# Kernel optimization log

Measured on AMD Instinct MI355X. Metric: run time of the kernel, lower is better.

The kernel has to match this reference:

```python
import jax, jax.numpy as jnp
import numpy as np

GROUP_NUMS = 30
T_ITERS = 10
SIGMA = 0.01
SEED_THRESHOLD = 0.1


def _gumbel_topk(key, logits, k):
    # Sampling without replacement (torch.multinomial replacement=False) via Gumbel-top-k.
    u = jax.random.uniform(key, logits.shape, minval=1e-9, maxval=1.0)
    g = -jnp.log(-jnp.log(u))
    return jax.lax.top_k(logits + g, k)[1]


def _pairwise_dist(x):
    # x: [B,3,S] -> [B,S,S]
    return jnp.linalg.norm(x[:, :, :, None] - x[:, :, None, :], axis=1)


def _one_iterate(key, src_xyz, src_corr_xyz, weights, seed_nums, group_nums):
    B, _, N = src_xyz.shape
    S, G = seed_nums, group_nums
    k1, k2 = jax.random.split(key)
    # seed sampling without replacement, proportional to weights
    seed_idx = _gumbel_topk(k1, jnp.log(weights), S)                       # [B,S]
    seed_w = jnp.take_along_axis(weights, seed_idx, axis=-1)              # [B,S]
    idx3 = jnp.broadcast_to(seed_idx[:, None, :], (B, 3, S))
    seed_src = jnp.take_along_axis(src_xyz, idx3, axis=-1)                # [B,3,S]
    seed_corr = jnp.take_along_axis(src_corr_xyz, idx3, axis=-1)          # [B,3,S]
    # geometric consensus (no_grad in torch)
    cons = jnp.exp(-(_pairwise_dist(seed_src) - _pairwise_dist(seed_corr)) ** 2 / SIGMA)
    cons = jax.lax.stop_gradient(jnp.clip(cons, 0.1, None))               # [B,S,S]
    probs = cons / jnp.sum(cons, axis=-1, keepdims=True)
    nn_idx = _gumbel_topk(k2, jnp.log(probs), G)                          # [B,S,G]
    bidx = jnp.arange(B)[:, None, None]
    src_pts = seed_src.transpose(0, 2, 1)                                 # [B,S,3]
    corr_pts = seed_corr.transpose(0, 2, 1)
    src_nn = src_pts[bidx, nn_idx]                                        # [B,S,G,3]
    corr_nn = corr_pts[bidx, nn_idx]                                      # [B,S,G,3]
    w_nn = seed_w[bidx, nn_idx]                                           # [B,S,G]
    src2 = src_nn.transpose(0, 1, 3, 2).reshape(B * S, 3, G)
    corr2 = corr_nn.transpose(0, 1, 3, 2).reshape(B * S, 3, G)
    w2 = w_nn.reshape(B * S, G)
    w2 = w2 / jnp.sum(w2, axis=-1, keepdims=True)
    src_c = src2 - src2.mean(axis=2, keepdims=True)
    corr_c = corr2 - corr2.mean(axis=2, keepdims=True)
    H = jnp.matmul(src_c * w2[:, None, :], corr_c.transpose(0, 2, 1))     # [BS,3,3]
    U, _, Vh = jnp.linalg.svd(H)
    V = Vh.transpose(0, 2, 1)          # torch.svd returns V (not V^T)
    Ut = U.transpose(0, 2, 1)
    detv = jnp.linalg.det(jnp.matmul(V, Ut))                              # [BS]
    d = jnp.stack([jnp.ones_like(detv), jnp.ones_like(detv), detv], axis=-1)
    R = jnp.matmul(V * d[:, None, :], Ut)                                 # V @ diag(1,1,det) @ U^T
    t = jnp.matmul(-R, src2.mean(axis=2, keepdims=True)) + corr2.mean(axis=2, keepdims=True)  # [BS,3,1]
    R = R.reshape(B, S, 3, 3)
    t = t.reshape(B, S, 1, 3)
    pred = jnp.einsum('bsnm,bmk->bsnk', R, src_xyz) + t.transpose(0, 1, 3, 2)  # [B,S,3,N]
    L2 = jnp.linalg.norm(pred - src_corr_xyz[:, None, :, :], axis=-2)     # [B,S,N]
    fitness = jnp.mean((L2 < SEED_THRESHOLD).astype(jnp.float32), axis=-1)  # [B,S]
    best = jnp.argmax(fitness, axis=-1)                                   # [B]
    vv = jnp.mean(jnp.max(fitness, axis=-1))
    ba = jnp.arange(B)
    return vv, R[ba, best], t[ba, best]


def setup_inputs() -> dict:
    key = jax.random.key(0)
    k1, k2, k3 = jax.random.split(key, 3)
    B, N = 8, 2048
    src_xyz = jax.random.normal(k1, (B, 3, N), dtype=jnp.float32)
    tgt_xyz = jax.random.normal(k2, (B, 3, N), dtype=jnp.float32)
    weights = jax.random.normal(k3, (B, N), dtype=jnp.float32)
    return {"src_xyz": src_xyz, "tgt_xyz": tgt_xyz, "weights": weights}


def reference(src_xyz, tgt_xyz, weights):
    key = jax.random.key(42)
    w = jnp.where(jnp.isnan(weights), jnp.float32(1e-7), weights)
    w = jnp.where(jnp.isinf(w), jnp.float32(1.0), w)
    seed_nums = w.shape[-1] // 2
    w = jax.nn.softmax(w, axis=-1)
    B = src_xyz.shape[0]
    dist = jnp.float32(1e8)
    Rs = jnp.zeros((B, 3, 3), jnp.float32)
    ts = jnp.zeros((B, 1, 3), jnp.float32)
    for it in range(T_ITERS):
        vv, fR, ft = _one_iterate(jax.random.fold_in(key, it), src_xyz, tgt_xyz, w, seed_nums, GROUP_NUMS)
        better = vv < dist
        Rs = jnp.where(better, fR, Rs)
        ts = jnp.where(better, ft, ts)
        dist = jnp.where(better, vv, dist)
    return Rs, ts[:, 0, :]
```

## Files before the change

kernel.cpp:

```cpp
#include <hip/hip_runtime.h>
#include <stdint.h>
#include <math.h>

#pragma clang fp contract(off)

#define NB    8
#define NPTS  2048
#define NS    1024
#define NG    30
#define NITER 10

typedef unsigned long long ull;

__host__ __device__ __forceinline__ uint32_t rotl32(uint32_t x, int r){
  return (x << r) | (x >> (32 - r));
}
__host__ __device__ __forceinline__ void tf2x32(uint32_t k0, uint32_t k1,
                                                uint32_t x0, uint32_t x1,
                                                uint32_t& o0, uint32_t& o1){
  uint32_t k2 = k0 ^ k1 ^ 0x1BD11BDAu;
  x0 += k0; x1 += k1;
#define TFR(r) { x0 += x1; x1 = rotl32(x1, (r)); x1 ^= x0; }
  TFR(13) TFR(15) TFR(26) TFR(6)
  x0 += k1; x1 += k2 + 1u;
  TFR(17) TFR(29) TFR(16) TFR(24)
  x0 += k2; x1 += k0 + 2u;
  TFR(13) TFR(15) TFR(26) TFR(6)
  x0 += k0; x1 += k1 + 3u;
  TFR(17) TFR(29) TFR(16) TFR(24)
  x0 += k1; x1 += k2 + 4u;
  TFR(13) TFR(15) TFR(26) TFR(6)
  x0 += k2; x1 += k0 + 5u;
#undef TFR
  o0 = x0; o1 = x1;
}

__device__ __forceinline__ uint32_t rand_bits(uint32_t k0, uint32_t k1, uint32_t e){
  uint32_t o0, o1; tf2x32(k0, k1, 0u, e, o0, o1);
  return o0 ^ o1;
}

__device__ __forceinline__ void derive_key(int it, uint32_t which,
                                           uint32_t& a, uint32_t& b){
  uint32_t fa, fb;
  tf2x32(0u, 42u, 0u, (uint32_t)it, fa, fb);
  tf2x32(fa, fb, 0u, which, a, b);
}

__device__ __forceinline__ float gumbel_from(uint32_t bits){
  float f = __uint_as_float((bits >> 9) | 0x3f800000u) - 1.0f;
  float u = fmaxf(1e-9f, f + 1e-9f);
  return -logf(-logf(u));
}

__device__ __forceinline__ ull packkey(float v, uint32_t idx){
  uint32_t u = __float_as_uint(v);
  u = (u & 0x80000000u) ? ~u : (u | 0x80000000u);
  return ((ull)u << 32) | (ull)(0xFFFFFFFFu - idx);
}
__device__ __forceinline__ uint32_t unpackidx(ull k){
  return 0xFFFFFFFFu - (uint32_t)(k & 0xFFFFFFFFull);
}

__device__ __forceinline__ void bitonic_desc(ull* a, int M, int t, int T){
  for (int k = 2; k <= M; k <<= 1){
    for (int j = k >> 1; j > 0; j >>= 1){
      for (int i = t; i < M; i += T){
        int ixj = i ^ j;
        if (ixj > i){
          ull ai = a[i], aj = a[ixj];
          bool desc = ((i & k) == 0);
          if (desc ? (ai < aj) : (ai > aj)){ a[i] = aj; a[ixj] = ai; }
        }
      }
      __syncthreads();
    }
  }
}

__device__ __forceinline__ ull shfl_xor_u64(ull x, int mask){
  return (ull)__shfl_xor((long long)x, mask, 64);
}

__device__ __forceinline__ ull sort32_desc(ull key, int l){
  int i = l & 31;
#pragma unroll
  for (int k = 2; k <= 16; k <<= 1){
#pragma unroll
    for (int j = k >> 1; j > 0; j >>= 1){
      ull other = shfl_xor_u64(key, j);
      bool up = ((l & j) == 0);
      bool take_max = (((i & k) == 0) == up);
      bool omax = other > key;
      key = (take_max == omax) ? other : key;
    }
  }
#pragma unroll
  for (int j = 16; j > 0; j >>= 1){
    ull other = shfl_xor_u64(key, j);
    bool up = ((l & j) == 0);
    bool omax = other > key;
    key = (up == omax) ? other : key;
  }
  return key;
}

__device__ __forceinline__ ull merge64_desc(ull key, int l){
#pragma unroll
  for (int j = 32; j > 0; j >>= 1){
    ull other = shfl_xor_u64(key, j);
    bool up = ((l & j) == 0);
    bool omax = other > key;
    key = (up == omax) ? other : key;
  }
  return key;
}

__device__ __forceinline__ ull mergehalves_desc(ull key, int l){
  ull rev = shfl_xor_u64(key, 31);
  if (l >= 32) key = rev;
  return merge64_desc(key, l);
}

__global__ __launch_bounds__(256) void ghv_softmax(const float* __restrict__ win,
                                                   float* __restrict__ w,
                                                   float* __restrict__ logw){
  int b = blockIdx.x, t = threadIdx.x;
  __shared__ float sh[NPTS];
  __shared__ float red[4];
  __shared__ float bcast;
  for (int n = t; n < NPTS; n += 256){
    float x = win[b*NPTS + n];
    if (isnan(x)) x = 1e-7f;
    if (isinf(x)) x = 1.0f;
    sh[n] = x;
  }
  __syncthreads();
  float m = -INFINITY;
  for (int n = t; n < NPTS; n += 256) m = fmaxf(m, sh[n]);
  for (int off = 32; off >= 1; off >>= 1) m = fmaxf(m, __shfl_down(m, off));
  if ((t & 63) == 0) red[t >> 6] = m;
  __syncthreads();
  if (t == 0) bcast = fmaxf(fmaxf(red[0], red[1]), fmaxf(red[2], red[3]));
  __syncthreads();
  float mx = bcast;
  float ss = 0.0f;
  for (int n = t; n < NPTS; n += 256){ float e = expf(sh[n] - mx); sh[n] = e; ss += e; }
  for (int off = 32; off >= 1; off >>= 1) ss += __shfl_down(ss, off);
  if ((t & 63) == 0) red[t >> 6] = ss;
  __syncthreads();
  if (t == 0) bcast = red[0] + red[1] + red[2] + red[3];
  __syncthreads();
  float tot = bcast;
  for (int n = t; n < NPTS; n += 256){
    float wv = sh[n] / tot;
    w[b*NPTS + n] = wv;
    logw[b*NPTS + n] = logf(wv);
  }
}

__global__ __launch_bounds__(1024) void ghv_seed(const float* __restrict__ src,
                                                 const float* __restrict__ tgt,
                                                 const float* __restrict__ w,
                                                 const float* __restrict__ logw,
                                                 float* __restrict__ seeds,
                                                 int it0, int seq){
  __shared__ ull keys[NPTS];
  __shared__ uint32_t kk[2];
  int b = blockIdx.x, t = threadIdx.x;
  int it = it0 + blockIdx.z;
  int slot = seq ? 0 : it;
  if (t == 0){ derive_key(it, 0u, kk[0], kk[1]); }
  __syncthreads();
  uint32_t k0 = kk[0], k1 = kk[1];
  for (int n = t; n < NPTS; n += 1024){
    uint32_t bits = rand_bits(k0, k1, (uint32_t)(b*NPTS + n));
    float v = logw[b*NPTS + n] + gumbel_from(bits);
    keys[n] = packkey(v, (uint32_t)n);
  }
  __syncthreads();
  bitonic_desc(keys, NPTS, t, 1024);
  int s = t;
  uint32_t idx = unpackidx(keys[s]);
  const float* sb = src + b*3*NPTS;
  const float* tb = tgt + b*3*NPTS;
  float* sp = seeds + (size_t)slot*(NB*NS*8) + (size_t)((b << 10) + s) * 8;
  sp[0] = sb[idx]; sp[1] = sb[NPTS + idx]; sp[2] = sb[2*NPTS + idx];
  sp[3] = tb[idx]; sp[4] = tb[NPTS + idx]; sp[5] = tb[2*NPTS + idx];
  sp[6] = w[b*NPTS + idx]; sp[7] = 0.0f;
}

__global__ __launch_bounds__(512) void ghv_nn(const float* __restrict__ seeds,
                                              unsigned short* __restrict__ nnb,
                                              int it0, int seq){
  __shared__ float red[8];
  __shared__ float srow[8];
  __shared__ float rowsum_sh;
  __shared__ float cmax[32];
  __shared__ float Tsh;
  __shared__ int cnt_sh;
  __shared__ uint32_t kk[2];
  __shared__ ull kbuf[NS];
  __shared__ ull sbuf[256];
  __shared__ ull sbuf2[128];

  int s = blockIdx.x, b = blockIdx.y, t = threadIdx.x;
  int it = it0 + blockIdx.z;
  int slot = seq ? 0 : it;
  const float* sdat = seeds + (size_t)slot*(NB*NS*8);
  size_t outoff = ((size_t)slot*(NB*NS) + (size_t)((b << 10) + s))*32;
  int wv = t >> 6, l = t & 63;

  if (t < 8) srow[t] = sdat[(size_t)((b << 10) + s)*8 + t];
  if (t == 0){ derive_key(it, 1u, kk[0], kk[1]); cnt_sh = 0; }
  __syncthreads();
  uint32_t k0 = kk[0], k1 = kk[1];

  float consr[2];
  float part = 0.0f;
#pragma unroll
  for (int q = 0; q < 2; ++q){
    int j = t + q*512;
    const float4* jp = (const float4*)(sdat + (size_t)((b << 10) + j)*8);
    float4 p0 = jp[0], p1 = jp[1];
    float dxs = srow[0]-p0.x, dys = srow[1]-p0.y, dzs = srow[2]-p0.z;
    float ds  = sqrtf(dxs*dxs + dys*dys + dzs*dzs);
    float dxc = srow[3]-p0.w, dyc = srow[4]-p1.x, dzc = srow[5]-p1.y;
    float dc  = sqrtf(dxc*dxc + dyc*dyc + dzc*dzc);
    float diff = ds - dc;
    float cons = expf((-(diff*diff)) / 0.01f);
    cons = fmaxf(cons, 0.1f);
    consr[q] = cons;
    part += cons;
  }
  for (int off = 32; off >= 1; off >>= 1) part += __shfl_down(part, off);
  if ((t & 63) == 0) red[t >> 6] = part;
  __syncthreads();
  if (t == 0){ float tot = 0.0f; for (int i = 0; i < 8; ++i) tot += red[i]; rowsum_sh = tot; }
  __syncthreads();
  float rowsum = rowsum_sh;

  float v0, v1; ull key0, key1;
  {
    int e = t;
    uint32_t bits = rand_bits(k0, k1, (uint32_t)((b << 20) + (s << 10) + e));
    v0 = logf(consr[0] / rowsum) + gumbel_from(bits);
    key0 = packkey(v0, (uint32_t)e);
  }
  {
    int e = t + 512;
    uint32_t bits = rand_bits(k0, k1, (uint32_t)((b << 20) + (s << 10) + e));
    v1 = logf(consr[1] / rowsum) + gumbel_from(bits);
    key1 = packkey(v1, (uint32_t)e);
  }

  {
    float cm0 = v0;
#pragma unroll
    for (int j = 1; j <= 16; j <<= 1) cm0 = fmaxf(cm0, __shfl_xor(cm0, j));
    if ((l & 31) == 0) cmax[(wv << 1) + (l >> 5)] = cm0;
    float cm1 = v1;
#pragma unroll
    for (int j = 1; j <= 16; j <<= 1) cm1 = fmaxf(cm1, __shfl_xor(cm1, j));
    if ((l & 31) == 0) cmax[16 + (wv << 1) + (l >> 5)] = cm1;
  }
  __syncthreads();
  if (t < 32){
    float m = cmax[t];
#pragma unroll
    for (int j = 1; j <= 16; j <<= 1) m = fminf(m, __shfl_xor(m, j));
    if (t == 0) Tsh = m;
  }
  __syncthreads();
  float T = Tsh;

  bool kp0 = (v0 >= T), kp1 = (v1 >= T);
  ull b0m = __ballot(kp0), b1m = __ballot(kp1);
  int c0 = __popcll(b0m);
  int base = 0;
  if (l == 0) base = atomicAdd(&cnt_sh, c0 + __popcll(b1m));
  base = __shfl(base, 0);
  ull ltm = (l == 0) ? 0ull : ((1ull << l) - 1ull);
  if (kp0) kbuf[base + __popcll(b0m & ltm)] = key0;
  if (kp1) kbuf[base + c0 + __popcll(b1m & ltm)] = key1;
  __syncthreads();
  int n = cnt_sh;

  if (n <= 512){
    if (t >= n) kbuf[t] = 0ull;
    __syncthreads();
    ull key = 0ull;
    if (wv * 64 < n){
      key = kbuf[t];
      key = sort32_desc(key, l);
      key = mergehalves_desc(key, l);
    }
    if (l < 32) sbuf[(wv << 5) + l] = key;
    __syncthreads();
    if (wv < 4){
      ull k2 = 0ull;
      if (wv * 128 < n){
        k2 = (l < 32) ? sbuf[(wv << 6) + l] : sbuf[(wv << 6) + 95 - l];
        k2 = merge64_desc(k2, l);
      }
      if (l < 32) sbuf2[(wv << 5) + l] = k2;
    }
    __syncthreads();
    if (wv < 2){
      ull k2 = (l < 32) ? sbuf2[(wv << 6) + l] : sbuf2[(wv << 6) + 95 - l];
      k2 = merge64_desc(k2, l);
      if (l < 32) sbuf[(wv << 5) + l] = k2;
    }
    __syncthreads();
    if (wv == 0){
      ull k2 = (l < 32) ? sbuf[l] : sbuf[95 - l];
      k2 = merge64_desc(k2, l);
      if (l < 32){
        unsigned short vidx = (l < NG) ? (unsigned short)unpackidx(k2) : 0;
        nnb[outoff + l] = vidx;
      }
    }
  } else {
    kbuf[t] = key0;
    kbuf[t + 512] = key1;
    __syncthreads();
    bitonic_desc(kbuf, NS, t, 512);
    if (t < 32){
      unsigned short vidx = (t < NG) ? (unsigned short)unpackidx(kbuf[t]) : 0;
      nnb[outoff + t] = vidx;
    }
  }
}

__global__ __launch_bounds__(64) void ghv_kabsch(const float* __restrict__ seeds,
                                                 const unsigned short* __restrict__ nnb,
                                                 float* __restrict__ Rt,
                                                 int it0, int seq){
  int id = blockIdx.x*64 + threadIdx.x;
  int it = it0 + blockIdx.z;
  int slot = seq ? 0 : it;
  int b = id >> 10;
  const float* sdat = seeds + (size_t)slot*(NB*NS*8);
  const unsigned short* nnp = nnb + ((size_t)slot*(NB*NS) + (size_t)id)*32;

  float sxs=0, sys=0, szs=0, cxs=0, cys=0, czs=0, wsum=0;
  for (int g = 0; g < NG; ++g){
    int j = nnp[g];
    const float4* jp = (const float4*)(sdat + (size_t)((b << 10) + j)*8);
    float4 p0 = jp[0], p1 = jp[1];
    sxs += p0.x; sys += p0.y; szs += p0.z;
    cxs += p0.w; cys += p1.x; czs += p1.y;
    wsum += p1.z;
  }
  float msx = sxs/30.0f, msy = sys/30.0f, msz = szs/30.0f;
  float mcx = cxs/30.0f, mcy = cys/30.0f, mcz = czs/30.0f;

  float Hf[9] = {0,0,0,0,0,0,0,0,0};
  for (int g = 0; g < NG; ++g){
    int j = nnp[g];
    const float4* jp = (const float4*)(sdat + (size_t)((b << 10) + j)*8);
    float4 p0 = jp[0], p1 = jp[1];
    float wg = p1.z / wsum;
    float a0 = p0.x - msx, a1 = p0.y - msy, a2 = p0.z - msz;
    float b0 = p0.w - mcx, b1 = p1.x - mcy, b2 = p1.y - mcz;
    float a0w = a0*wg, a1w = a1*wg, a2w = a2*wg;
    Hf[0] += a0w*b0; Hf[1] += a0w*b1; Hf[2] += a0w*b2;
    Hf[3] += a1w*b0; Hf[4] += a1w*b1; Hf[5] += a1w*b2;
    Hf[6] += a2w*b0; Hf[7] += a2w*b1; Hf[8] += a2w*b2;
  }

  double H[9]; for (int i = 0; i < 9; ++i) H[i] = (double)Hf[i];
  double A[3][3];
  A[0][0] = H[0]*H[0] + H[3]*H[3] + H[6]*H[6];
  A[0][1] = H[0]*H[1] + H[3]*H[4] + H[6]*H[7];
  A[0][2] = H[0]*H[2] + H[3]*H[5] + H[6]*H[8];
  A[1][1] = H[1]*H[1] + H[4]*H[4] + H[7]*H[7];
  A[1][2] = H[1]*H[2] + H[4]*H[5] + H[7]*H[8];
  A[2][2] = H[2]*H[2] + H[5]*H[5] + H[8]*H[8];
  A[1][0] = A[0][1]; A[2][0] = A[0][2]; A[2][1] = A[1][2];
  double V[3][3] = {{1,0,0},{0,1,0},{0,0,1}};
  for (int sw = 0; sw < 12; ++sw){
    for (int p = 0; p < 2; ++p){
      for (int q = p+1; q < 3; ++q){
        double apq = A[p][q];
        if (fabs(apq) > 1e-300){
          double th = (A[q][q] - A[p][p]) / (2.0*apq);
          double tt = copysign(1.0, th) / (fabs(th) + sqrt(1.0 + th*th));
          double c  = 1.0 / sqrt(1.0 + tt*tt), sn = tt*c;
          int r = 3 - p - q;
          double app = A[p][p], aqq = A[q][q];
          double arp = A[r][p], arq = A[r][q];
          A[p][p] = app - tt*apq;
          A[q][q] = aqq + tt*apq;
          A[p][q] = 0.0; A[q][p] = 0.0;
          A[r][p] = c*arp - sn*arq; A[p][r] = A[r][p];
          A[r][q] = sn*arp + c*arq; A[q][r] = A[r][q];
          for (int kk = 0; kk < 3; ++kk){
            double vp = V[kk][p], vq = V[kk][q];
            V[kk][p] = c*vp - sn*vq;
            V[kk][q] = sn*vp + c*vq;
          }
        }
      }
    }
  }
  int o0 = 0, o1 = 1, o2 = 2;
  double l0 = A[0][0], l1 = A[1][1], l2 = A[2][2];
  double tmp; int ti;
  if (l0 < l1){ tmp=l0; l0=l1; l1=tmp; ti=o0; o0=o1; o1=ti; }
  if (l0 < l2){ tmp=l0; l0=l2; l2=tmp; ti=o0; o0=o2; o2=ti; }
  if (l1 < l2){ tmp=l1; l1=l2; l2=tmp; ti=o1; o1=o2; o2=ti; }
  double v0[3] = {V[0][o0], V[1][o0], V[2][o0]};
  double v1[3] = {V[0][o1], V[1][o1], V[2][o1]};
  double v2[3] = {V[0][o2], V[1][o2], V[2][o2]};

  double u0[3], u1[3], u2[3];
  for (int i = 0; i < 3; ++i) u0[i] = H[i*3+0]*v0[0] + H[i*3+1]*v0[1] + H[i*3+2]*v0[2];
  double n0 = sqrt(u0[0]*u0[0] + u0[1]*u0[1] + u0[2]*u0[2]);
  if (n0 > 1e-150){ u0[0]/=n0; u0[1]/=n0; u0[2]/=n0; }
  else { u0[0]=1; u0[1]=0; u0[2]=0; }
  for (int i = 0; i < 3; ++i) u1[i] = H[i*3+0]*v1[0] + H[i*3+1]*v1[1] + H[i*3+2]*v1[2];
  double d01 = u0[0]*u1[0] + u0[1]*u1[1] + u0[2]*u1[2];
  for (int i = 0; i < 3; ++i) u1[i] -= d01*u0[i];
  double n1 = sqrt(u1[0]*u1[0] + u1[1]*u1[1] + u1[2]*u1[2]);
  if (n1 > 1e-150){ u1[0]/=n1; u1[1]/=n1; u1[2]/=n1; }
  else {
    double ax = fabs(u0[0]), ay = fabs(u0[1]), az = fabs(u0[2]);
    double e[3] = {0,0,0};
    if (ax <= ay && ax <= az) e[0] = 1; else if (ay <= az) e[1] = 1; else e[2] = 1;
    double de = u0[0]*e[0] + u0[1]*e[1] + u0[2]*e[2];
    for (int i = 0; i < 3; ++i) u1[i] = e[i] - de*u0[i];
    double nn1 = sqrt(u1[0]*u1[0] + u1[1]*u1[1] + u1[2]*u1[2]);
    for (int i = 0; i < 3; ++i) u1[i] /= nn1;
  }
  u2[0] = u0[1]*u1[2] - u0[2]*u1[1];
  u2[1] = u0[2]*u1[0] - u0[0]*u1[2];
  u2[2] = u0[0]*u1[1] - u0[1]*u1[0];
  double detV = v0[0]*(v1[1]*v2[2] - v1[2]*v2[1])
              - v0[1]*(v1[0]*v2[2] - v1[2]*v2[0])
              + v0[2]*(v1[0]*v2[1] - v1[1]*v2[0]);
  float Rf[9];
  for (int i = 0; i < 3; ++i)
    for (int j = 0; j < 3; ++j)
      Rf[i*3+j] = (float)(v0[i]*u0[j] + v1[i]*u1[j] + detV*(v2[i]*u2[j]));
  float tx = -(Rf[0]*msx + Rf[1]*msy + Rf[2]*msz) + mcx;
  float ty = -(Rf[3]*msx + Rf[4]*msy + Rf[5]*msz) + mcy;
  float tz = -(Rf[6]*msx + Rf[7]*msy + Rf[8]*msz) + mcz;
  float* o = Rt + ((size_t)slot*(NB*NS) + (size_t)id)*12;
  for (int i = 0; i < 9; ++i) o[i] = Rf[i];
  o[9] = tx; o[10] = ty; o[11] = tz;
}

__global__ __launch_bounds__(256) void ghv_fitness(const float* __restrict__ src,
                                                   const float* __restrict__ tgt,
                                                   const float* __restrict__ Rt,
                                                   int* __restrict__ fit){
  __shared__ float Pf[12288];
  int b = blockIdx.y, t = threadIdx.x;
  int slot = blockIdx.z;
  int s0 = blockIdx.x * 16;
  const float4* g4s = (const float4*)(src + (size_t)b*3*NPTS);
  const float4* g4t = (const float4*)(tgt + (size_t)b*3*NPTS);
  float4* l4 = (float4*)Pf;
  for (int i = t; i < 1536; i += 256){
    l4[i] = g4s[i];
    l4[1536 + i] = g4t[i];
  }
  __syncthreads();
  int wv = t >> 6, l = t & 63;
  for (int k = 0; k < 4; ++k){
    int s = s0 + wv*4 + k;
    size_t id = (size_t)slot*(NB*NS) + (size_t)((b << 10) + s);
    const float* rt = Rt + id*12;
    float R0 = rt[0], R1 = rt[1], R2 = rt[2];
    float R3 = rt[3], R4 = rt[4], R5 = rt[5];
    float R6 = rt[6], R7 = rt[7], R8 = rt[8];
    float t0 = rt[9], t1 = rt[10], t2 = rt[11];
    int cnt = 0;
    for (int n = l; n < NPTS; n += 64){
      float x = Pf[n], y = Pf[2048 + n], z = Pf[4096 + n];
      float px = R0*x + R1*y + R2*z + t0;
      float py = R3*x + R4*y + R5*z + t1;
      float pz = R6*x + R7*y + R8*z + t2;
      float dx = px - Pf[6144 + n], dy = py - Pf[8192 + n], dz = pz - Pf[10240 + n];
      float l2 = sqrtf(dx*dx + dy*dy + dz*dz);
      cnt += (l2 < 0.1f) ? 1 : 0;
    }
    for (int off = 32; off >= 1; off >>= 1) cnt += __shfl_down(cnt, off);
    if (l == 0) fit[id] = cnt;
  }
}

__global__ __launch_bounds__(512) void ghv_select_b(const float* __restrict__ Rt,
                                                    const int* __restrict__ fit,
                                                    float* __restrict__ out){
  __shared__ int mc[NITER*NB], mi[NITER*NB];
  __shared__ int best_sh;
  int t = threadIdx.x;
  int w = t >> 6, l = t & 63;
  for (int task = w; task < NITER*NB; task += 8){
    int it = task >> 3, b = task & 7;
    int bc = -1, bi = 0;
    const int* fp = fit + (size_t)it*(NB*NS) + (b << 10);
    for (int s = l; s < NS; s += 64){
      int c = fp[s];
      if (c > bc){ bc = c; bi = s; }
    }
    for (int off = 32; off >= 1; off >>= 1){
      int oc = __shfl_down(bc, off);
      int oi = __shfl_down(bi, off);
      if (oc > bc || (oc == bc && oi < bi)){ bc = oc; bi = oi; }
    }
    if (l == 0){ mc[task] = bc; mi[task] = bi; }
  }
  __syncthreads();
  if (t == 0){
    float dist = 1e8f;
    int best = 0;
    for (int it = 0; it < NITER; ++it){
      int sum = 0;
      for (int b = 0; b < NB; ++b) sum += mc[(it << 3) + b];
      float vv = (float)sum / 16384.0f;
      if (vv < dist){ dist = vv; best = it; }
    }
    best_sh = best;
  }
  __syncthreads();
  int bit = best_sh;
  for (int i = t; i < 96; i += 512){
    float v;
    if (i < 72){
      int bb = i / 9, k = i % 9;
      v = Rt[((size_t)bit*(NB*NS) + (size_t)((bb << 10) + mi[(bit << 3) + bb]))*12 + k];
    } else {
      int ii = i - 72; int bb = ii / 3, k = ii % 3;
      v = Rt[((size_t)bit*(NB*NS) + (size_t)((bb << 10) + mi[(bit << 3) + bb]))*12 + 9 + k];
    }
    out[i] = v;
  }
}

__global__ __launch_bounds__(512) void ghv_select_s(const float* __restrict__ Rt,
                                                    const int* __restrict__ fit,
                                                    float* __restrict__ dist_ws,
                                                    float* __restrict__ out,
                                                    int first){
  __shared__ int mc[8], mi[8];
  __shared__ int flag;
  int t = threadIdx.x;
  int b = t >> 6, lane = t & 63;
  int bc = -1, bi = 0;
  for (int s = lane; s < NS; s += 64){
    int c = fit[(b << 10) + s];
    if (c > bc){ bc = c; bi = s; }
  }
  for (int off = 32; off >= 1; off >>= 1){
    int oc = __shfl_down(bc, off);
    int oi = __shfl_down(bi, off);
    if (oc > bc || (oc == bc && oi < bi)){ bc = oc; bi = oi; }
  }
  if (lane == 0){ mc[b] = bc; mi[b] = bi; }
  __syncthreads();
  if (t == 0){
    int sum = 0; for (int i = 0; i < 8; ++i) sum += mc[i];
    float vv = (float)sum / 16384.0f;
    float dist = first ? 1e8f : dist_ws[0];
    int better = (vv < dist) ? 1 : 0;
    if (better) dist_ws[0] = vv;
    flag = better;
  }
  __syncthreads();
  if (flag){
    for (int i = t; i < 96; i += 512){
      float v;
      if (i < 72){
        int bb = i / 9, k = i % 9;
        v = Rt[(size_t)((bb << 10) + mi[bb])*12 + k];
      } else {
        int ii = i - 72; int bb = ii / 3, k = ii % 3;
        v = Rt[(size_t)((bb << 10) + mi[bb])*12 + 9 + k];
      }
      out[i] = v;
    }
  }
}

extern "C" void kernel_launch(void* const* d_in, const int* in_sizes, int n_in,
                              void* d_out, int out_size, void* d_ws, size_t ws_size,
                              hipStream_t stream){
  const float* src = (const float*)d_in[0];
  const float* tgt = (const float*)d_in[1];
  const float* win = (const float*)d_in[2];
  float* out = (float*)d_out;
  char* ws = (char*)d_ws;

  const size_t SEEDS_SZ = (size_t)NB*NS*8*4;
  const size_t RT_SZ    = (size_t)NB*NS*12*4;
  const size_t NN_SZ    = (size_t)NB*NS*32*2;
  const size_t FIT_SZ   = (size_t)NB*NS*4;
  const size_t W_SZ     = (size_t)NB*NPTS*4;

  size_t off_w    = 0;
  size_t off_logw = off_w + W_SZ;
  size_t off_seed = off_logw + W_SZ;
  size_t off_Rt   = off_seed + NITER*SEEDS_SZ;
  size_t off_nn   = off_Rt + NITER*RT_SZ;
  size_t off_fit  = off_nn + NITER*NN_SZ;
  size_t need_b   = off_fit + NITER*FIT_SZ;

  if (ws_size >= need_b){
    float* w     = (float*)(ws + off_w);
    float* logw  = (float*)(ws + off_logw);
    float* seeds = (float*)(ws + off_seed);
    float* Rt    = (float*)(ws + off_Rt);
    unsigned short* nnb = (unsigned short*)(ws + off_nn);
    int*   fit   = (int*)(ws + off_fit);

    ghv_softmax<<<NB, 256, 0, stream>>>(win, w, logw);
    ghv_seed   <<<dim3(NB, 1, NITER), 1024, 0, stream>>>(src, tgt, w, logw, seeds, 0, 0);
    ghv_nn     <<<dim3(NS, NB, NITER), 512, 0, stream>>>(seeds, nnb, 0, 0);
    ghv_kabsch <<<dim3(NB*NS/64, 1, NITER), 64, 0, stream>>>(seeds, nnb, Rt, 0, 0);
    ghv_fitness<<<dim3(NS/16, NB, NITER), 256, 0, stream>>>(src, tgt, Rt, fit);
    ghv_select_b<<<1, 512, 0, stream>>>(Rt, fit, out);
  } else {
    size_t o_w = 0, o_lw = W_SZ, o_sd = 2*W_SZ, o_rt = o_sd + SEEDS_SZ,
           o_nn2 = o_rt + RT_SZ, o_ft = o_nn2 + NN_SZ, o_ds = o_ft + FIT_SZ;
    float* w     = (float*)(ws + o_w);
    float* logw  = (float*)(ws + o_lw);
    float* seeds = (float*)(ws + o_sd);
    float* Rt    = (float*)(ws + o_rt);
    unsigned short* nnb = (unsigned short*)(ws + o_nn2);
    int*   fit   = (int*)(ws + o_ft);
    float* dist  = (float*)(ws + o_ds);

    ghv_softmax<<<NB, 256, 0, stream>>>(win, w, logw);
    for (int it = 0; it < NITER; ++it){
      ghv_seed   <<<dim3(NB, 1, 1), 1024, 0, stream>>>(src, tgt, w, logw, seeds, it, 1);
      ghv_nn     <<<dim3(NS, NB, 1), 512, 0, stream>>>(seeds, nnb, it, 1);
      ghv_kabsch <<<dim3(NB*NS/64, 1, 1), 64, 0, stream>>>(seeds, nnb, Rt, it, 1);
      ghv_fitness<<<dim3(NS/16, NB, 1), 256, 0, stream>>>(src, tgt, Rt, fit);
      ghv_select_s<<<1, 512, 0, stream>>>(Rt, fit, dist, out, (it == 0) ? 1 : 0);
    }
  }
}
```

Baseline: 933.0 us.

## Sort 64-key runs in registers, halve Jacobi sweeps, widen fitness blocks

The seed kernel now sorts each 64-element run inside a wavefront with register shuffles (sort32_desc and mergehalves_desc) before the shared-memory bitonic merge stages, which removes the early barrier-heavy sort stages. The Jacobi eigen-solve in Kabsch drops from 12 to 6 sweeps. This trims per-thread double-precision work but risks less converged rotations on hard inputs. The fitness kernel handles 32 hypotheses per block instead of 16, so the shared-memory load of the point cloud is amortised over more hypotheses, with half as many blocks.

```diff
diff --git a/kernel.cpp b/kernel.cpp
--- a/kernel.cpp
+++ b/kernel.cpp
@@ -173,13 +173,33 @@
   if (t == 0){ derive_key(it, 0u, kk[0], kk[1]); }
   __syncthreads();
   uint32_t k0 = kk[0], k1 = kk[1];
-  for (int n = t; n < NPTS; n += 1024){
-    uint32_t bits = rand_bits(k0, k1, (uint32_t)(b*NPTS + n));
-    float v = logw[b*NPTS + n] + gumbel_from(bits);
-    keys[n] = packkey(v, (uint32_t)n);
-  }
-  __syncthreads();
-  bitonic_desc(keys, NPTS, t, 1024);
+  int wv = t >> 6, l = t & 63;
+#pragma unroll
+  for (int p = 0; p < 2; ++p){
+    int j = (wv << 1) + p;
+    int e = (j << 6) + l;
+    uint32_t bits = rand_bits(k0, k1, (uint32_t)(b*NPTS + e));
+    float v = logw[b*NPTS + e] + gumbel_from(bits);
+    ull key = packkey(v, (uint32_t)e);
+    key = sort32_desc(key, l);
+    key = mergehalves_desc(key, l);
+    if (j & 1) key = shfl_xor_u64(key, 63);
+    keys[e] = key;
+  }
+  __syncthreads();
+  for (int k = 128; k <= NPTS; k <<= 1){
+    for (int j2 = k >> 1; j2 > 0; j2 >>= 1){
+      for (int i = t; i < NPTS; i += 1024){
+        int ixj = i ^ j2;
+        if (ixj > i){
+          ull ai = keys[i], aj = keys[ixj];
+          bool desc = ((i & k) == 0);
+          if (desc ? (ai < aj) : (ai > aj)){ keys[i] = aj; keys[ixj] = ai; }
+        }
+      }
+      __syncthreads();
+    }
+  }
   int s = t;
   uint32_t idx = unpackidx(keys[s]);
   const float* sb = src + b*3*NPTS;
@@ -379,7 +399,7 @@
   A[2][2] = H[2]*H[2] + H[5]*H[5] + H[8]*H[8];
   A[1][0] = A[0][1]; A[2][0] = A[0][2]; A[2][1] = A[1][2];
   double V[3][3] = {{1,0,0},{0,1,0},{0,0,1}};
-  for (int sw = 0; sw < 12; ++sw){
+  for (int sw = 0; sw < 6; ++sw){
     for (int p = 0; p < 2; ++p){
       for (int q = p+1; q < 3; ++q){
         double apq = A[p][q];
@@ -458,7 +478,7 @@
   __shared__ float Pf[12288];
   int b = blockIdx.y, t = threadIdx.x;
   int slot = blockIdx.z;
-  int s0 = blockIdx.x * 16;
+  int s0 = blockIdx.x * 32;
   const float4* g4s = (const float4*)(src + (size_t)b*3*NPTS);
   const float4* g4t = (const float4*)(tgt + (size_t)b*3*NPTS);
   float4* l4 = (float4*)Pf;
@@ -468,8 +488,8 @@
   }
   __syncthreads();
   int wv = t >> 6, l = t & 63;
-  for (int k = 0; k < 4; ++k){
-    int s = s0 + wv*4 + k;
+  for (int k = 0; k < 8; ++k){
+    int s = s0 + wv*8 + k;
     size_t id = (size_t)slot*(NB*NS) + (size_t)((b << 10) + s);
     const float* rt = Rt + id*12;
     float R0 = rt[0], R1 = rt[1], R2 = rt[2];
@@ -620,7 +640,7 @@
     ghv_seed   <<<dim3(NB, 1, NITER), 1024, 0, stream>>>(src, tgt, w, logw, seeds, 0, 0);
     ghv_nn     <<<dim3(NS, NB, NITER), 512, 0, stream>>>(seeds, nnb, 0, 0);
     ghv_kabsch <<<dim3(NB*NS/64, 1, NITER), 64, 0, stream>>>(seeds, nnb, Rt, 0, 0);
-    ghv_fitness<<<dim3(NS/16, NB, NITER), 256, 0, stream>>>(src, tgt, Rt, fit);
+    ghv_fitness<<<dim3(NS/32, NB, NITER), 256, 0, stream>>>(src, tgt, Rt, fit);
     ghv_select_b<<<1, 512, 0, stream>>>(Rt, fit, out);
   } else {
     size_t o_w = 0, o_lw = W_SZ, o_sd = 2*W_SZ, o_rt = o_sd + SEEDS_SZ,
@@ -638,7 +658,7 @@
       ghv_seed   <<<dim3(NB, 1, 1), 1024, 0, stream>>>(src, tgt, w, logw, seeds, it, 1);
       ghv_nn     <<<dim3(NS, NB, 1), 512, 0, stream>>>(seeds, nnb, it, 1);
       ghv_kabsch <<<dim3(NB*NS/64, 1, 1), 64, 0, stream>>>(seeds, nnb, Rt, it, 1);
-      ghv_fitness<<<dim3(NS/16, NB, 1), 256, 0, stream>>>(src, tgt, Rt, fit);
+      ghv_fitness<<<dim3(NS/32, NB, 1), 256, 0, stream>>>(src, tgt, Rt, fit);
       ghv_select_s<<<1, 512, 0, stream>>>(Rt, fit, dist, out, (it == 0) ? 1 : 0);
     }
   }
```

Measured after the change: 953.2 us. 1.02x slower.
